# Kernel tuning notes

Hardware: AMD Instinct MI355X
Metric: run time of the kernel (lower is better)

Reference implementation:

```python
import jax, jax.numpy as jnp
import numpy as np

EPS = 1e-5

def _ln(x, g, b):
    mu = jnp.mean(x, axis=-1, keepdims=True)
    var = jnp.mean(jnp.square(x - mu), axis=-1, keepdims=True)
    return (x - mu) * jax.lax.rsqrt(var + EPS) * g + b


def setup_inputs() -> dict:
    key = jax.random.key(0)
    ks = jax.random.split(key, 16)
    B, T, D, H = 8, 4096, 512, 1024
    s_d = 1.0 / np.sqrt(D)
    s_h = 1.0 / np.sqrt(H)
    return {
        "x": jax.random.normal(ks[0], (B, T, D), dtype=jnp.float32),
        "gamma": jnp.ones((D,), jnp.float32),
        "beta": jnp.zeros((D,), jnp.float32),
        "Wq": jax.random.uniform(ks[1], (D, H), jnp.float32, -s_d, s_d),
        "bq": jax.random.uniform(ks[2], (H,), jnp.float32, -s_d, s_d),
        "Wk": jax.random.uniform(ks[3], (D, H), jnp.float32, -s_d, s_d),
        "bk": jax.random.uniform(ks[4], (H,), jnp.float32, -s_d, s_d),
        "Wv": jax.random.uniform(ks[5], (D, H), jnp.float32, -s_d, s_d),
        "bv": jax.random.uniform(ks[6], (H,), jnp.float32, -s_d, s_d),
        "wbias": jax.random.uniform(ks[7], (H,), jnp.float32, 0.0, 1.0),
        "Wo": jax.random.uniform(ks[8], (H, D), jnp.float32, -s_h, s_h),
        "bo": jax.random.uniform(ks[9], (D,), jnp.float32, -s_h, s_h),
        "W1": jax.random.uniform(ks[10], (D, H), jnp.float32, -s_d, s_d),
        "b1": jax.random.uniform(ks[11], (H,), jnp.float32, -s_d, s_d),
        "W2": jax.random.uniform(ks[12], (H, D), jnp.float32, -s_h, s_h),
        "b2": jax.random.uniform(ks[13], (D,), jnp.float32, -s_h, s_h),
    }


def reference(x, gamma, beta, Wq, bq, Wk, bk, Wv, bv, wbias, Wo, bo, W1, b1, W2, b2):
    # --- pre-LN ---
    x1 = _ln(x, gamma, beta)                      # [B,T,D]
    # --- AFTFull attention (NOTE: sums over BATCH dim 0, as in original repo) ---
    Q = jnp.einsum('btd,dh->bth', x1, Wq) + bq    # [B,T,H]
    K = jnp.einsum('btd,dh->bth', x1, Wk) + bk
    V = jnp.einsum('btd,dh->bth', x1, Wv) + bv
    Q_sig = jax.nn.sigmoid(Q)
    numer = jnp.exp(K + wbias)                    # [B,T,H]
    denom = jnp.sum(numer, axis=0)                # [T,H]
    weighted = jnp.sum(numer * V, axis=0) / denom # [T,H]
    Yt = Q_sig * weighted                         # [B,T,H] (broadcast)
    Yt = jnp.einsum('bth,hd->btd', Yt, Wo) + bo   # [B,T,D]
    x2 = Yt + x1                                  # residual (dropout = identity, eval)
    # --- second LN (same params, as in original) + MLP ---
    x3 = _ln(x2, gamma, beta)
    h = jax.nn.gelu(jnp.einsum('btd,dh->bth', x3, W1) + b1, approximate=False)
    m = jnp.einsum('bth,hd->btd', h, W2) + b2
    # original: out = dropout(m) + m  ==  2*m at eval (no residual to x2)
    return m + m
```

## Files before the change

kernel.cpp:

```cpp
#include <hip/hip_runtime.h>
#include <hip/hip_bf16.h>
#include <cstdint>

using u16 = unsigned short;
using u32 = unsigned int;

typedef __bf16 bf16x8 __attribute__((ext_vector_type(8)));
typedef float  f32x4  __attribute__((ext_vector_type(4)));

#define DEV static __device__ __forceinline__

DEV float bf2f(u16 u){ union { u32 u; float f; } c; c.u = ((u32)u) << 16; return c.f; }

DEV u16 f2bf(float f){
  __bf16 h = (__bf16)f;
  return __builtin_bit_cast(u16, h);
}

DEV float fast_rcp(float x){ return __builtin_amdgcn_rcpf(x); }

DEV void async16(const u16* g, u16* l){
  __builtin_amdgcn_global_load_lds((const __attribute__((address_space(1))) u32*)g,
                                   (__attribute__((address_space(3))) u32*)l,
                                   16, 0, 0);
}

#define BARRIER() __builtin_amdgcn_s_barrier()
#define LGKM0() do { __asm__ volatile("s_waitcnt lgkmcnt(0)" ::: "memory"); \
                     __builtin_amdgcn_sched_barrier(0); } while (0)
#define VMCNT(n) __asm__ volatile("s_waitcnt vmcnt(" #n ")" ::: "memory")

__global__ __launch_bounds__(256)
void prep_fused(const float* __restrict__ W0, const float* __restrict__ W1,
                const float* __restrict__ W2, const float* __restrict__ W3,
                const float* __restrict__ W4, const float* __restrict__ W5,
                u16* __restrict__ T0, u16* __restrict__ T1, u16* __restrict__ T2,
                u16* __restrict__ T3, u16* __restrict__ T4, u16* __restrict__ T5,
                const float* __restrict__ x, const float* __restrict__ gamma,
                const float* __restrict__ beta, u16* __restrict__ x1b){
  const int z = blockIdx.z;
  if (z >= 6){
    const int bid = (z - 6) * 1024 + blockIdx.y * 32 + blockIdx.x;
    const int tid = threadIdx.y * 32 + threadIdx.x;
    const int wid = tid >> 6;
    const int lane = tid & 63;
    const size_t row = (size_t)bid * 4 + wid;
    const int d0 = lane * 8;
    const float* xp = x + row * 512 + d0;
    float4 p0 = *(const float4*)xp;
    float4 p1 = *(const float4*)(xp + 4);
    float v[8] = {p0.x,p0.y,p0.z,p0.w,p1.x,p1.y,p1.z,p1.w};
    float s = 0.f, sq = 0.f;
    #pragma unroll
    for (int i = 0; i < 8; ++i){ s += v[i]; sq += v[i]*v[i]; }
    #pragma unroll
    for (int o = 32; o >= 1; o >>= 1){ s += __shfl_xor(s, o); sq += __shfl_xor(sq, o); }
    const float mu  = s * (1.0f/512.0f);
    const float var = sq * (1.0f/512.0f) - mu*mu;
    const float rstd = rsqrtf(var + 1e-5f);
    const float4 g0 = *(const float4*)(gamma + d0);
    const float4 g1 = *(const float4*)(gamma + d0 + 4);
    const float4 b0 = *(const float4*)(beta + d0);
    const float4 b1 = *(const float4*)(beta + d0 + 4);
    float gg[8] = {g0.x,g0.y,g0.z,g0.w,g1.x,g1.y,g1.z,g1.w};
    float bb[8] = {b0.x,b0.y,b0.z,b0.w,b1.x,b1.y,b1.z,b1.w};
    u16 o8[8];
    #pragma unroll
    for (int i = 0; i < 8; ++i)
      o8[i] = f2bf((v[i]-mu)*rstd*gg[i] + bb[i]);
    *(uint4*)(x1b + row*512 + d0) = *(const uint4*)o8;
    return;
  }
  const float* W; u16* WT; int R, C;
  switch (z){
    case 0:  W = W0; WT = T0; R = 512;  C = 1024; break;
    case 1:  W = W1; WT = T1; R = 512;  C = 1024; break;
    case 2:  W = W2; WT = T2; R = 512;  C = 1024; break;
    case 3:  W = W3; WT = T3; R = 1024; C = 512;  break;
    case 4:  W = W4; WT = T4; R = 512;  C = 1024; break;
    default: W = W5; WT = T5; R = 1024; C = 512;  break;
  }
  const int c0 = blockIdx.x * 32, r0 = blockIdx.y * 32;
  if (c0 >= C || r0 >= R) return;
  __shared__ float tile[32][33];
  const int tx = threadIdx.x, ty = threadIdx.y;
  #pragma unroll
  for (int j = 0; j < 4; ++j)
    tile[ty + j*8][tx] = W[(size_t)(r0 + ty + j*8) * C + (c0 + tx)];
  __syncthreads();
  #pragma unroll
  for (int j = 0; j < 4; ++j)
    WT[(size_t)(c0 + ty + j*8) * R + (r0 + tx)] = f2bf(tile[tx][ty + j*8]);
}

template<bool BF16IN>
__global__ __launch_bounds__(256)
void ln_kernel(const void* __restrict__ xin, const float* __restrict__ gamma,
               const float* __restrict__ beta, u16* __restrict__ xout){
  const int wid = threadIdx.x >> 6;
  const int lane = threadIdx.x & 63;
  const size_t row = (size_t)blockIdx.x * 4 + wid;
  const int d0 = lane * 8;
  float v[8];
  if constexpr (BF16IN){
    const u16* xp = (const u16*)xin + row * 512 + d0;
    uint4 p = *(const uint4*)xp;
    const u16* s = (const u16*)&p;
    #pragma unroll
    for (int i = 0; i < 8; ++i) v[i] = bf2f(s[i]);
  } else {
    const float* xp = (const float*)xin + row * 512 + d0;
    float4 p0 = *(const float4*)xp;
    float4 p1 = *(const float4*)(xp + 4);
    v[0]=p0.x; v[1]=p0.y; v[2]=p0.z; v[3]=p0.w;
    v[4]=p1.x; v[5]=p1.y; v[6]=p1.z; v[7]=p1.w;
  }
  float s = 0.f, sq = 0.f;
  #pragma unroll
  for (int i = 0; i < 8; ++i){ s += v[i]; sq += v[i]*v[i]; }
  #pragma unroll
  for (int o = 32; o >= 1; o >>= 1){ s += __shfl_xor(s, o); sq += __shfl_xor(sq, o); }
  const float mu  = s * (1.0f/512.0f);
  const float var = sq * (1.0f/512.0f) - mu*mu;
  const float rstd = rsqrtf(var + 1e-5f);
  const float4 g0 = *(const float4*)(gamma + d0);
  const float4 g1 = *(const float4*)(gamma + d0 + 4);
  const float4 b0 = *(const float4*)(beta + d0);
  const float4 b1 = *(const float4*)(beta + d0 + 4);
  float gg[8] = {g0.x,g0.y,g0.z,g0.w,g1.x,g1.y,g1.z,g1.w};
  float bb[8] = {b0.x,b0.y,b0.z,b0.w,b1.x,b1.y,b1.z,b1.w};
  u16 o8[8];
  #pragma unroll
  for (int i = 0; i < 8; ++i)
    o8[i] = f2bf((v[i]-mu)*rstd*gg[i] + bb[i]);
  *(uint4*)(xout + row*512 + d0) = *(const uint4*)o8;
}

__global__ __launch_bounds__(256)
void aft_fused(const u16* __restrict__ numer, const u16* __restrict__ V,
               const u16* __restrict__ qs, u16* __restrict__ yt){
  const size_t TH = (size_t)4096 * 1024;
  const size_t i8 = ((size_t)blockIdx.x * 256 + threadIdx.x) * 8;
  float den[8], ws[8];
  #pragma unroll
  for (int j = 0; j < 8; ++j){ den[j] = 0.f; ws[j] = 0.f; }
  #pragma unroll
  for (int b = 0; b < 8; ++b){
    uint4 pn = *(const uint4*)(numer + b*TH + i8);
    uint4 pv = *(const uint4*)(V     + b*TH + i8);
    const u16* n = (const u16*)&pn;
    const u16* v = (const u16*)&pv;
    #pragma unroll
    for (int j = 0; j < 8; ++j){ float nf = bf2f(n[j]); den[j] += nf; ws[j] += nf * bf2f(v[j]); }
  }
  float w[8];
  #pragma unroll
  for (int j = 0; j < 8; ++j) w[j] = ws[j] * fast_rcp(den[j]);
  #pragma unroll
  for (int b = 0; b < 8; ++b){
    uint4 pq = *(const uint4*)(qs + b*TH + i8);
    const u16* q = (const u16*)&pq;
    u16 o[8];
    #pragma unroll
    for (int j = 0; j < 8; ++j) o[j] = f2bf(bf2f(q[j]) * w[j]);
    *(uint4*)(yt + b*TH + i8) = *(const uint4*)o;
  }
}

template<int EPI, int KC>
__global__ __launch_bounds__(256, 3)
void gemm128(const u16* __restrict__ A, const u16* __restrict__ Bt, int nTiles,
             const float* __restrict__ bias0, const float* __restrict__ wbias,
             u16* __restrict__ out0, u16* __restrict__ out1, u16* __restrict__ out2,
             const float* __restrict__ bias1, const float* __restrict__ bias2,
             const u16* __restrict__ resid, float* __restrict__ outf){
  __shared__ u16 ldsA[128*64];
  __shared__ u16 ldsB[128*64];
  const int tid  = threadIdx.x;
  const int wid  = tid >> 6;
  const int lane = tid & 63;
  const int quad = lane >> 4;
  const int lr   = lane & 15;

  const int lin = blockIdx.x;
  const int GS  = 16 * nTiles;
  const int g   = lin / GS;
  const int rem = lin - g * GS;
  const int tileM = (g * 16 + (rem & 15)) * 128;
  const int tileN = (rem >> 4) * 128;

  const int wmBase = (wid & 1) * 64;
  const int wnBase = (wid >> 1) * 64;

  f32x4 acc[4][4] = {};

  int srow[4], scb[4];
  #pragma unroll
  for (int r = 0; r < 4; ++r){
    const int off = r*4096 + wid*1024 + lane*16;
    srow[r] = off >> 7;
    scb[r]  = ((off >> 4) & 7) ^ (srow[r] & 7);
  }
  const u16* aSrc[4]; const u16* bSrc[4];
  #pragma unroll
  for (int r = 0; r < 4; ++r){
    aSrc[r] = A  + (size_t)(tileM + srow[r]) * KC + scb[r]*8;
    bSrc[r] = Bt + (size_t)(tileN + srow[r]) * KC + scb[r]*8;
  }

  int aOff[2][4], bOff[2][4];
  #pragma unroll
  for (int s = 0; s < 2; ++s)
    #pragma unroll
    for (int i = 0; i < 4; ++i){
      const int m = wmBase + i*16 + lr;
      const int n = wnBase + i*16 + lr;
      aOff[s][i] = m*128 + (((s*4 + quad) ^ (m & 7)) * 16);
      bOff[s][i] = n*128 + (((s*4 + quad) ^ (n & 7)) * 16);
    }

  #pragma unroll
  for (int kt = 0; kt < KC; kt += 64){
    #pragma unroll
    for (int r = 0; r < 4; ++r){
      async16(aSrc[r] + kt, (u16*)((char*)ldsA + r*4096 + wid*1024));
      async16(bSrc[r] + kt, (u16*)((char*)ldsB + r*4096 + wid*1024));
    }
    __syncthreads();
    #pragma unroll
    for (int s = 0; s < 2; ++s){
      bf16x8 ar[4], br[4];
      #pragma unroll
      for (int i = 0; i < 4; ++i) ar[i] = *(const bf16x8*)((const char*)ldsA + aOff[s][i]);
      #pragma unroll
      for (int i = 0; i < 4; ++i) br[i] = *(const bf16x8*)((const char*)ldsB + bOff[s][i]);
      #pragma unroll
      for (int i = 0; i < 4; ++i)
        #pragma unroll
        for (int j = 0; j < 4; ++j)
          acc[i][j] = __builtin_amdgcn_mfma_f32_16x16x32_bf16(br[j], ar[i], acc[i][j], 0, 0, 0);
    }
    __syncthreads();
  }

  if (EPI == 3){
    #pragma unroll
    for (int j = 0; j < 4; ++j){
      const int colb = tileN + wnBase + j*16 + quad*4;
      const float4 bvv = *(const float4*)(bias0 + colb);
      #pragma unroll
      for (int i = 0; i < 4; ++i){
        const int row = tileM + wmBase + i*16 + lr;
        float4 o;
        #pragma unroll
        for (int r = 0; r < 4; ++r)
          ((float*)&o)[r] = 2.0f * (acc[i][j][r] + ((const float*)&bvv)[r]);
        *(float4*)(outf + (size_t)row * 512 + colb) = o;
      }
    }
    return;
  }

  u16* eb = ldsA + wid * 1152;
  const int mat = (EPI == 0) ? (tileN >> 10) : 0;
  const float* biasP = bias0;
  u16* outP = out0;
  int ldO = 1024, cb0 = tileN + wnBase;
  if (EPI == 0){
    biasP = (mat==0) ? bias0 : (mat==1) ? bias1 : bias2;
    outP  = (mat==0) ? out0  : (mat==1) ? out1  : out2;
    cb0   = (tileN & 1023) + wnBase;
  } else if (EPI == 1){
    ldO = 512;
  }

  #pragma unroll
  for (int i = 0; i < 4; ++i){
    const int row = tileM + wmBase + i*16 + lr;
    #pragma unroll
    for (int j = 0; j < 4; ++j){
      const int cl = j*16 + quad*4;
      const float4 bvv = *(const float4*)(biasP + cb0 + cl);
      u16 o[4];
      if (EPI == 0){
        float4 wbv = {0,0,0,0};
        if (mat == 1) wbv = *(const float4*)(wbias + cb0 + cl);
        #pragma unroll
        for (int r = 0; r < 4; ++r){
          float v = acc[i][j][r] + ((const float*)&bvv)[r];
          if (mat == 0)      v = fast_rcp(1.0f + __expf(-v));
          else if (mat == 1) v = __expf(v + ((const float*)&wbv)[r]);
          o[r] = f2bf(v);
        }
      } else if (EPI == 1){
        uint2 pr = *(const uint2*)(resid + (size_t)row * 512 + cb0 + cl);
        const u16* rp = (const u16*)&pr;
        #pragma unroll
        for (int r = 0; r < 4; ++r)
          o[r] = f2bf(acc[i][j][r] + ((const float*)&bvv)[r] + bf2f(rp[r]));
      } else {
        #pragma unroll
        for (int r = 0; r < 4; ++r){
          float v = acc[i][j][r] + ((const float*)&bvv)[r];
          float u2 = 2.0f * v * (0.7978845608f + 0.0356774081f * v * v);
          float t  = 1.0f - 2.0f * fast_rcp(1.0f + __expf(u2));
          o[r] = f2bf(0.5f * v * (1.0f + t));
        }
      }
      *(uint2*)(eb + lr*72 + cl) = *(const uint2*)o;
    }
    __asm__ volatile("s_waitcnt lgkmcnt(0)" ::: "memory");
    uint4 p0 = *(const uint4*)(eb + lr*72 + quad*16);
    uint4 p1 = *(const uint4*)(eb + lr*72 + quad*16 + 8);
    __asm__ volatile("s_waitcnt lgkmcnt(0)" ::: "memory");
    u16* gp = outP + (size_t)row * ldO + cb0 + quad*16;
    *(uint4*)gp = p0;
    *(uint4*)(gp + 8) = p1;
  }
}

template<int EPI, int KC>
__global__ __launch_bounds__(512, 2)
void gemm256(const u16* __restrict__ A, const u16* __restrict__ Bt,
             const float* __restrict__ bias0, const float* __restrict__ wbias,
             u16* __restrict__ out0, u16* __restrict__ out1, u16* __restrict__ out2,
             const float* __restrict__ bias1, const float* __restrict__ bias2,
             const u16* __restrict__ resid, float* __restrict__ outf){
  constexpr int NK = KC / 64;
  __shared__ __align__(16) char smem[65536];

  const int tid  = threadIdx.x;
  const int wid  = tid >> 6;
  const int lane = tid & 63;
  const int quad = lane >> 4;
  const int lr   = lane & 15;
  const int wm   = wid & 1;
  const int wn   = wid >> 1;

  const int nwg = gridDim.x;
  const int wg  = (blockIdx.x & 7) * (nwg >> 3) + (blockIdx.x >> 3);
  const int nNT = nwg >> 7;
  const int sgs = nNT << 2;
  const int sg  = wg / sgs;
  const int r   = wg - sg * sgs;
  const int tileM = (sg*4 + (r & 3)) * 256;
  const int tileN = (r >> 2) * 256;

  const u16* sA[2][2]; const u16* sB[2][2];
  {
    const int off0 = wid*1024 + lane*16;
    #pragma unroll
    for (int rr_ = 0; rr_ < 2; ++rr_){
      const int off = rr_*8192 + off0;
      const int rr  = off >> 7;
      const int g   = (((off >> 4) & 7) ^ (rr & 7)) * 8;
      #pragma unroll
      for (int h = 0; h < 2; ++h){
        sA[h][rr_] = A  + (size_t)(tileM + (rr>>6)*128 + h*64 + (rr&63)) * KC + g;
        sB[h][rr_] = Bt + (size_t)(tileN + (rr>>5)*64  + h*32 + (rr&31)) * KC + g;
      }
    }
  }
  auto stA = [&](int h, int kt){
    char* d = smem + h*16384 + wid*1024;
    async16(sA[h][0] + kt, (u16*)d);
    async16(sA[h][1] + kt, (u16*)(d + 8192));
  };
  auto stB = [&](int h, int kt){
    char* d = smem + 32768 + h*16384 + wid*1024;
    async16(sB[h][0] + kt, (u16*)d);
    async16(sB[h][1] + kt, (u16*)(d + 8192));
  };

  const int cO0  = ((quad)     ^ (lr & 7)) * 16;
  const int cO1  = ((quad ^ 4) ^ (lr & 7)) * 16;
  const int aRow = (wm*64 + lr) * 128;
  const int bRow = (wn*32 + lr) * 128;

  bf16x8 ar[4][2], br0[2][2], br1[2][2];
  f32x4 acc[2][2][4][2] = {};

  auto ldA = [&](int mh){
    #pragma unroll
    for (int i = 0; i < 4; ++i){
      ar[i][0] = *(const bf16x8*)(smem + mh*16384 + aRow + i*2048 + cO0);
      ar[i][1] = *(const bf16x8*)(smem + mh*16384 + aRow + i*2048 + cO1);
    }
  };
  auto ldB = [&](int nh, bf16x8 (&br)[2][2]){
    #pragma unroll
    for (int j = 0; j < 2; ++j){
      br[j][0] = *(const bf16x8*)(smem + 32768 + nh*16384 + bRow + j*2048 + cO0);
      br[j][1] = *(const bf16x8*)(smem + 32768 + nh*16384 + bRow + j*2048 + cO1);
    }
  };
  auto MF = [&](int mh, int nh, bf16x8 (&br)[2][2]){
    __builtin_amdgcn_s_setprio(1);
    #pragma unroll
    for (int i = 0; i < 4; ++i)
      #pragma unroll
      for (int j = 0; j < 2; ++j){
        acc[mh][nh][i][j] = __builtin_amdgcn_mfma_f32_16x16x32_bf16(br[j][0], ar[i][0], acc[mh][nh][i][j], 0, 0, 0);
        acc[mh][nh][i][j] = __builtin_amdgcn_mfma_f32_16x16x32_bf16(br[j][1], ar[i][1], acc[mh][nh][i][j], 0, 0, 0);
      }
    __builtin_amdgcn_s_setprio(0);
  };

  stA(0, 0); stB(0, 0); stB(1, 0); stA(1, 0);
  VMCNT(4);
  BARRIER();

  #pragma unroll 1
  for (int t = 0; t < NK-1; ++t){
    const int kt = (t+1)*64;
    ldA(0); ldB(0, br0);
    BARRIER(); LGKM0();
    MF(0, 0, br0);
    VMCNT(2);
    BARRIER();
    ldB(1, br1);
    stA(0, kt); stB(0, kt);
    BARRIER(); LGKM0();
    MF(0, 1, br1);
    VMCNT(4);
    BARRIER();
    ldA(1);
    stB(1, kt);
    BARRIER(); LGKM0();
    MF(1, 1, br1);
    BARRIER();
    stA(1, kt);
    MF(1, 0, br0);
    VMCNT(4);
    BARRIER();
  }
  ldA(0); ldB(0, br0);
  BARRIER(); LGKM0();
  MF(0, 0, br0);
  VMCNT(2);
  BARRIER();
  ldB(1, br1);
  BARRIER(); LGKM0();
  MF(0, 1, br1);
  VMCNT(0);
  BARRIER();
  ldA(1);
  BARRIER(); LGKM0();
  MF(1, 1, br1);
  BARRIER();
  MF(1, 0, br0);

  if (EPI == 3){
    #pragma unroll
    for (int mh = 0; mh < 2; ++mh)
    #pragma unroll
    for (int i = 0; i < 4; ++i){
      const int row = tileM + wm*128 + mh*64 + i*16 + lr;
      #pragma unroll
      for (int nh = 0; nh < 2; ++nh)
      #pragma unroll
      for (int j = 0; j < 2; ++j){
        const int colb = tileN + wn*64 + nh*32 + j*16 + quad*4;
        const float4 bvv = *(const float4*)(bias0 + colb);
        float4 o;
        #pragma unroll
        for (int r_ = 0; r_ < 4; ++r_)
          ((float*)&o)[r_] = 2.0f * (acc[mh][nh][i][j][r_] + ((const float*)&bvv)[r_]);
        *(float4*)(outf + (size_t)row * 512 + colb) = o;
      }
    }
    return;
  }

  char* eb = smem + wid * 2304;
  const int mat = 0;
  const float* biasP = bias0;
  u16* outP = out0;
  int ldO = 1024, cb0 = tileN + wn*64;
  if (EPI == 1){
    ldO = 512;
  }
  (void)mat;

  #pragma unroll
  for (int mh = 0; mh < 2; ++mh)
  #pragma unroll
  for (int i = 0; i < 4; ++i){
    const int row = tileM + wm*128 + mh*64 + i*16 + lr;
    #pragma unroll
    for (int nh = 0; nh < 2; ++nh)
    #pragma unroll
    for (int j = 0; j < 2; ++j){
      const int cl = (nh*2 + j)*16 + quad*4;
      const float4 bvv = *(const float4*)(biasP + cb0 + cl);
      u16 o[4];
      if (EPI == 1){
        uint2 pr = *(const uint2*)(resid + (size_t)row * 512 + cb0 + cl);
        const u16* rp = (const u16*)&pr;
        #pragma unroll
        for (int r_ = 0; r_ < 4; ++r_)
          o[r_] = f2bf(acc[mh][nh][i][j][r_] + ((const float*)&bvv)[r_] + bf2f(rp[r_]));
      } else {
        #pragma unroll
        for (int r_ = 0; r_ < 4; ++r_){
          float v  = acc[mh][nh][i][j][r_] + ((const float*)&bvv)[r_];
          float u2 = 2.0f * v * (0.7978845608f + 0.0356774081f * v * v);
          float tg = 1.0f - 2.0f * fast_rcp(1.0f + __expf(u2));
          o[r_] = f2bf(0.5f * v * (1.0f + tg));
        }
      }
      *(uint2*)(eb + lr*144 + cl*2) = *(const uint2*)o;
    }
    __asm__ volatile("s_waitcnt lgkmcnt(0)" ::: "memory");
    uint4 p0 = *(const uint4*)(eb + lr*144 + quad*32);
    uint4 p1 = *(const uint4*)(eb + lr*144 + quad*32 + 16);
    __asm__ volatile("s_waitcnt lgkmcnt(0)" ::: "memory");
    u16* gp = outP + (size_t)row * ldO + cb0 + quad*16;
    *(uint4*)gp = p0;
    *(uint4*)(gp + 8) = p1;
  }
}

extern "C" void kernel_launch(void* const* d_in, const int* in_sizes, int n_in,
                              void* d_out, int out_size, void* d_ws, size_t ws_size,
                              hipStream_t stream) {
  const float* x     = (const float*)d_in[0];
  const float* gamma = (const float*)d_in[1];
  const float* beta  = (const float*)d_in[2];
  const float* Wq    = (const float*)d_in[3];
  const float* bq    = (const float*)d_in[4];
  const float* Wk    = (const float*)d_in[5];
  const float* bk    = (const float*)d_in[6];
  const float* Wv    = (const float*)d_in[7];
  const float* bv    = (const float*)d_in[8];
  const float* wbias = (const float*)d_in[9];
  const float* Wo    = (const float*)d_in[10];
  const float* bo    = (const float*)d_in[11];
  const float* W1    = (const float*)d_in[12];
  const float* b1    = (const float*)d_in[13];
  const float* W2    = (const float*)d_in[14];
  const float* b2    = (const float*)d_in[15];
  float* out = (float*)d_out;

  char* w = (char*)d_ws;
  const size_t MB = 1ull << 20;
  u16* WqkvT = (u16*)(w + 0*MB);
  u16* WoT   = (u16*)(w + 3*MB);
  u16* W1T   = (u16*)(w + 4*MB);
  u16* W2T   = (u16*)(w + 5*MB);
  u16* x1b   = (u16*)(w + 6*MB);
  u16* Qs    = (u16*)(w + 38*MB);
  u16* Nu    = (u16*)(w + 102*MB);
  u16* Vb    = (u16*)(w + 166*MB);
  u16* Yt    = Nu;
  u16* x2b   = Vb;
  u16* x3b   = (u16*)(w + 198*MB);
  u16* hb    = Qs;

  prep_fused<<<dim3(32, 32, 14), dim3(32, 8), 0, stream>>>(
      Wq, Wk, Wv, Wo, W1, W2,
      WqkvT, WqkvT + 1024*512, WqkvT + 2*1024*512, WoT, W1T, W2T,
      x, gamma, beta, x1b);

  gemm128<0, 512><<<256*24, 256, 0, stream>>>(x1b, WqkvT, 24,
      bq, wbias, Qs, Nu, Vb, bk, bv, nullptr, nullptr);

  aft_fused<<<2048, 256, 0, stream>>>(Nu, Vb, Qs, Yt);

  gemm256<1, 1024><<<256, 512, 0, stream>>>(Yt, WoT,
      bo, nullptr, x2b, nullptr, nullptr, nullptr, nullptr, x1b, nullptr);

  ln_kernel<true><<<8192, 256, 0, stream>>>(x2b, gamma, beta, x3b);

  gemm256<2, 512><<<512, 512, 0, stream>>>(x3b, W1T,
      b1, nullptr, hb, nullptr, nullptr, nullptr, nullptr, nullptr, nullptr);

  gemm256<3, 1024><<<256, 512, 0, stream>>>(hb, W2T,
      b2, nullptr, nullptr, nullptr, nullptr, nullptr, nullptr, nullptr, out);
}
```

Baseline: 480.6 us.

## Fuse Q_sig*weighted product into Wo GEMM A-load and use 256-tile QKV GEMM

The AFT kernel now writes only the batch-reduced weighted [T,H] tensor, instead of reading Qs and writing a full [B,T,H] Yt. The Wo projection GEMM (gemm128_yt) loads Qs and Wt tiles into registers, multiplies them, and stores the product into LDS, so the Yt write and re-read go away. The QKV projection moves from gemm128 to the larger gemm256 with its EPI 0 epilogue, and the Wo GEMM moves from gemm256 to a 128 tile kernel with a non-unrolled K loop. The register-staged A path replaces async global-to-LDS loads for A and may expose load latency in the Wo GEMM.

```diff
diff --git a/kernel.cpp b/kernel.cpp
--- a/kernel.cpp
+++ b/kernel.cpp
@@ -137,8 +137,8 @@
 }
 
 __global__ __launch_bounds__(256)
-void aft_fused(const u16* __restrict__ numer, const u16* __restrict__ V,
-               const u16* __restrict__ qs, u16* __restrict__ yt){
+void aft_weighted(const u16* __restrict__ numer, const u16* __restrict__ V,
+                  u16* __restrict__ wt){
   const size_t TH = (size_t)4096 * 1024;
   const size_t i8 = ((size_t)blockIdx.x * 256 + threadIdx.x) * 8;
   float den[8], ws[8];
@@ -153,27 +153,17 @@
     #pragma unroll
     for (int j = 0; j < 8; ++j){ float nf = bf2f(n[j]); den[j] += nf; ws[j] += nf * bf2f(v[j]); }
   }
-  float w[8];
-  #pragma unroll
-  for (int j = 0; j < 8; ++j) w[j] = ws[j] * fast_rcp(den[j]);
-  #pragma unroll
-  for (int b = 0; b < 8; ++b){
-    uint4 pq = *(const uint4*)(qs + b*TH + i8);
-    const u16* q = (const u16*)&pq;
-    u16 o[8];
-    #pragma unroll
-    for (int j = 0; j < 8; ++j) o[j] = f2bf(bf2f(q[j]) * w[j]);
-    *(uint4*)(yt + b*TH + i8) = *(const uint4*)o;
-  }
-}
-
-template<int EPI, int KC>
+  u16 o[8];
+  #pragma unroll
+  for (int j = 0; j < 8; ++j) o[j] = f2bf(ws[j] * fast_rcp(den[j]));
+  *(uint4*)(wt + i8) = *(const uint4*)o;
+}
+
 __global__ __launch_bounds__(256, 3)
-void gemm128(const u16* __restrict__ A, const u16* __restrict__ Bt, int nTiles,
-             const float* __restrict__ bias0, const float* __restrict__ wbias,
-             u16* __restrict__ out0, u16* __restrict__ out1, u16* __restrict__ out2,
-             const float* __restrict__ bias1, const float* __restrict__ bias2,
-             const u16* __restrict__ resid, float* __restrict__ outf){
+void gemm128_yt(const u16* __restrict__ Qs, const u16* __restrict__ Bt, int nTiles,
+                const u16* __restrict__ Wt, const float* __restrict__ bias0,
+                u16* __restrict__ out0, const u16* __restrict__ resid){
+  constexpr int KC = 1024;
   __shared__ u16 ldsA[128*64];
   __shared__ u16 ldsB[128*64];
   const int tid  = threadIdx.x;
@@ -194,17 +184,20 @@
 
   f32x4 acc[4][4] = {};
 
-  int srow[4], scb[4];
+  int srow[4], cb[4], dOff[4], scb[4];
   #pragma unroll
   for (int r = 0; r < 4; ++r){
     const int off = r*4096 + wid*1024 + lane*16;
     srow[r] = off >> 7;
-    scb[r]  = ((off >> 4) & 7) ^ (srow[r] & 7);
-  }
-  const u16* aSrc[4]; const u16* bSrc[4];
+    cb[r]   = (off >> 4) & 7;
+    dOff[r] = srow[r]*128 + ((cb[r] ^ (srow[r] & 7)) << 4);
+    scb[r]  = cb[r] ^ (srow[r] & 7);
+  }
+  const u16* aSrc[4]; const u16* wSrc[4]; const u16* bSrc[4];
   #pragma unroll
   for (int r = 0; r < 4; ++r){
-    aSrc[r] = A  + (size_t)(tileM + srow[r]) * KC + scb[r]*8;
+    aSrc[r] = Qs + (size_t)(tileM + srow[r]) * KC + cb[r]*8;
+    wSrc[r] = Wt + (size_t)((tileM + srow[r]) & 4095) * 1024 + cb[r]*8;
     bSrc[r] = Bt + (size_t)(tileN + srow[r]) * KC + scb[r]*8;
   }
 
@@ -219,12 +212,24 @@
       bOff[s][i] = n*128 + (((s*4 + quad) ^ (n & 7)) * 16);
     }
 
-  #pragma unroll
+  #pragma unroll 1
   for (int kt = 0; kt < KC; kt += 64){
+    uint4 qa[4], wa[4];
+    #pragma unroll
+    for (int r = 0; r < 4; ++r) qa[r] = *(const uint4*)(aSrc[r] + kt);
+    #pragma unroll
+    for (int r = 0; r < 4; ++r) wa[r] = *(const uint4*)(wSrc[r] + kt);
+    #pragma unroll
+    for (int r = 0; r < 4; ++r)
+      async16(bSrc[r] + kt, (u16*)((char*)ldsB + r*4096 + wid*1024));
     #pragma unroll
     for (int r = 0; r < 4; ++r){
-      async16(aSrc[r] + kt, (u16*)((char*)ldsA + r*4096 + wid*1024));
-      async16(bSrc[r] + kt, (u16*)((char*)ldsB + r*4096 + wid*1024));
+      const u16* q = (const u16*)&qa[r];
+      const u16* wv = (const u16*)&wa[r];
+      u16 o[8];
+      #pragma unroll
+      for (int j = 0; j < 8; ++j) o[j] = f2bf(bf2f(q[j]) * bf2f(wv[j]));
+      *(uint4*)((char*)ldsA + dOff[r]) = *(const uint4*)o;
     }
     __syncthreads();
     #pragma unroll
@@ -243,77 +248,28 @@
     __syncthreads();
   }
 
-  if (EPI == 3){
-    #pragma unroll
-    for (int j = 0; j < 4; ++j){
-      const int colb = tileN + wnBase + j*16 + quad*4;
-      const float4 bvv = *(const float4*)(bias0 + colb);
-      #pragma unroll
-      for (int i = 0; i < 4; ++i){
-        const int row = tileM + wmBase + i*16 + lr;
-        float4 o;
-        #pragma unroll
-        for (int r = 0; r < 4; ++r)
-          ((float*)&o)[r] = 2.0f * (acc[i][j][r] + ((const float*)&bvv)[r]);
-        *(float4*)(outf + (size_t)row * 512 + colb) = o;
-      }
-    }
-    return;
-  }
-
   u16* eb = ldsA + wid * 1152;
-  const int mat = (EPI == 0) ? (tileN >> 10) : 0;
-  const float* biasP = bias0;
-  u16* outP = out0;
-  int ldO = 1024, cb0 = tileN + wnBase;
-  if (EPI == 0){
-    biasP = (mat==0) ? bias0 : (mat==1) ? bias1 : bias2;
-    outP  = (mat==0) ? out0  : (mat==1) ? out1  : out2;
-    cb0   = (tileN & 1023) + wnBase;
-  } else if (EPI == 1){
-    ldO = 512;
-  }
-
+  const int cb0 = tileN + wnBase;
   #pragma unroll
   for (int i = 0; i < 4; ++i){
     const int row = tileM + wmBase + i*16 + lr;
     #pragma unroll
     for (int j = 0; j < 4; ++j){
       const int cl = j*16 + quad*4;
-      const float4 bvv = *(const float4*)(biasP + cb0 + cl);
+      const float4 bvv = *(const float4*)(bias0 + cb0 + cl);
+      uint2 pr = *(const uint2*)(resid + (size_t)row * 512 + cb0 + cl);
+      const u16* rp = (const u16*)&pr;
       u16 o[4];
-      if (EPI == 0){
-        float4 wbv = {0,0,0,0};
-        if (mat == 1) wbv = *(const float4*)(wbias + cb0 + cl);
-        #pragma unroll
-        for (int r = 0; r < 4; ++r){
-          float v = acc[i][j][r] + ((const float*)&bvv)[r];
-          if (mat == 0)      v = fast_rcp(1.0f + __expf(-v));
-          else if (mat == 1) v = __expf(v + ((const float*)&wbv)[r]);
-          o[r] = f2bf(v);
-        }
-      } else if (EPI == 1){
-        uint2 pr = *(const uint2*)(resid + (size_t)row * 512 + cb0 + cl);
-        const u16* rp = (const u16*)&pr;
-        #pragma unroll
-        for (int r = 0; r < 4; ++r)
-          o[r] = f2bf(acc[i][j][r] + ((const float*)&bvv)[r] + bf2f(rp[r]));
-      } else {
-        #pragma unroll
-        for (int r = 0; r < 4; ++r){
-          float v = acc[i][j][r] + ((const float*)&bvv)[r];
-          float u2 = 2.0f * v * (0.7978845608f + 0.0356774081f * v * v);
-          float t  = 1.0f - 2.0f * fast_rcp(1.0f + __expf(u2));
-          o[r] = f2bf(0.5f * v * (1.0f + t));
-        }
-      }
+      #pragma unroll
+      for (int r = 0; r < 4; ++r)
+        o[r] = f2bf(acc[i][j][r] + ((const float*)&bvv)[r] + bf2f(rp[r]));
       *(uint2*)(eb + lr*72 + cl) = *(const uint2*)o;
     }
     __asm__ volatile("s_waitcnt lgkmcnt(0)" ::: "memory");
     uint4 p0 = *(const uint4*)(eb + lr*72 + quad*16);
     uint4 p1 = *(const uint4*)(eb + lr*72 + quad*16 + 8);
     __asm__ volatile("s_waitcnt lgkmcnt(0)" ::: "memory");
-    u16* gp = outP + (size_t)row * ldO + cb0 + quad*16;
+    u16* gp = out0 + (size_t)row * 512 + cb0 + quad*16;
     *(uint4*)gp = p0;
     *(uint4*)(gp + 8) = p1;
   }
@@ -325,7 +281,7 @@
              const float* __restrict__ bias0, const float* __restrict__ wbias,
              u16* __restrict__ out0, u16* __restrict__ out1, u16* __restrict__ out2,
              const float* __restrict__ bias1, const float* __restrict__ bias2,
-             const u16* __restrict__ resid, float* __restrict__ outf){
+             float* __restrict__ outf){
   constexpr int NK = KC / 64;
   __shared__ __align__(16) char smem[65536];
 
@@ -473,14 +429,15 @@
   }
 
   char* eb = smem + wid * 2304;
-  const int mat = 0;
+  const int mat = (EPI == 0) ? (tileN >> 10) : 0;
   const float* biasP = bias0;
   u16* outP = out0;
-  int ldO = 1024, cb0 = tileN + wn*64;
-  if (EPI == 1){
-    ldO = 512;
-  }
-  (void)mat;
+  int cb0 = tileN + wn*64;
+  if (EPI == 0){
+    biasP = (mat==0) ? bias0 : (mat==1) ? bias1 : bias2;
+    outP  = (mat==0) ? out0  : (mat==1) ? out1  : out2;
+    cb0   = (tileN & 1023) + wn*64;
+  }
 
   #pragma unroll
   for (int mh = 0; mh < 2; ++mh)
@@ -494,12 +451,16 @@
       const int cl = (nh*2 + j)*16 + quad*4;
       const float4 bvv = *(const float4*)(biasP + cb0 + cl);
       u16 o[4];
-      if (EPI == 1){
-        uint2 pr = *(const uint2*)(resid + (size_t)row * 512 + cb0 + cl);
-        const u16* rp = (const u16*)&pr;
+      if (EPI == 0){
+        float4 wbv = {0,0,0,0};
+        if (mat == 1) wbv = *(const float4*)(wbias + cb0 + cl);
         #pragma unroll
-        for (int r_ = 0; r_ < 4; ++r_)
-          o[r_] = f2bf(acc[mh][nh][i][j][r_] + ((const float*)&bvv)[r_] + bf2f(rp[r_]));
+        for (int r_ = 0; r_ < 4; ++r_){
+          float v = acc[mh][nh][i][j][r_] + ((const float*)&bvv)[r_];
+          if (mat == 0)      v = fast_rcp(1.0f + __expf(-v));
+          else if (mat == 1) v = __expf(v + ((const float*)&wbv)[r_]);
+          o[r_] = f2bf(v);
+        }
       } else {
         #pragma unroll
         for (int r_ = 0; r_ < 4; ++r_){
@@ -515,7 +476,7 @@
     uint4 p0 = *(const uint4*)(eb + lr*144 + quad*32);
     uint4 p1 = *(const uint4*)(eb + lr*144 + quad*32 + 16);
     __asm__ volatile("s_waitcnt lgkmcnt(0)" ::: "memory");
-    u16* gp = outP + (size_t)row * ldO + cb0 + quad*16;
+    u16* gp = outP + (size_t)row * 1024 + cb0 + quad*16;
     *(uint4*)gp = p0;
     *(uint4*)(gp + 8) = p1;
   }
@@ -552,7 +513,7 @@
   u16* Qs    = (u16*)(w + 38*MB);
   u16* Nu    = (u16*)(w + 102*MB);
   u16* Vb    = (u16*)(w + 166*MB);
-  u16* Yt    = Nu;
+  u16* Wt    = Nu;
   u16* x2b   = Vb;
   u16* x3b   = (u16*)(w + 198*MB);
   u16* hb    = Qs;
@@ -562,19 +523,18 @@
       WqkvT, WqkvT + 1024*512, WqkvT + 2*1024*512, WoT, W1T, W2T,
       x, gamma, beta, x1b);
 
-  gemm128<0, 512><<<256*24, 256, 0, stream>>>(x1b, WqkvT, 24,
-      bq, wbias, Qs, Nu, Vb, bk, bv, nullptr, nullptr);
-
-  aft_fused<<<2048, 256, 0, stream>>>(Nu, Vb, Qs, Yt);
-
-  gemm256<1, 1024><<<256, 512, 0, stream>>>(Yt, WoT,
-      bo, nullptr, x2b, nullptr, nullptr, nullptr, nullptr, x1b, nullptr);
+  gemm256<0, 512><<<1536, 512, 0, stream>>>(x1b, WqkvT,
+      bq, wbias, Qs, Nu, Vb, bk, bv, nullptr);
+
+  aft_weighted<<<2048, 256, 0, stream>>>(Nu, Vb, Wt);
+
+  gemm128_yt<<<1024, 256, 0, stream>>>(Qs, WoT, 4, Wt, bo, x2b, x1b);
 
   ln_kernel<true><<<8192, 256, 0, stream>>>(x2b, gamma, beta, x3b);
 
   gemm256<2, 512><<<512, 512, 0, stream>>>(x3b, W1T,
-      b1, nullptr, hb, nullptr, nullptr, nullptr, nullptr, nullptr, nullptr);
+      b1, nullptr, hb, nullptr, nullptr, nullptr, nullptr, nullptr);
 
   gemm256<3, 1024><<<256, 512, 0, stream>>>(hb, W2T,
-      b2, nullptr, nullptr, nullptr, nullptr, nullptr, nullptr, nullptr, out);
-}
+      b2, nullptr, nullptr, nullptr, nullptr, nullptr, nullptr, out);
+}
```

After: 475.4 us. About the same (-1.1%).
